# Kernel tuning notes

Measured on AMD Instinct MI355X. Metric: run time of the kernel, lower is better.

The kernel has to match this reference:

```python
import jax, jax.numpy as jnp
import numpy as np
import math

H = 14
W = 14
MU_MAX = math.sqrt((H / 2) ** 2 + (W / 2) ** 2)
EPS = 1e-6
LN_EPS = 1e-5


def _distance_sq():
    fy = np.fft.fftfreq(H) * H
    fx = np.fft.rfftfreq(W) * W
    d = fy[:, None] ** 2 + fx[None, :] ** 2  # (H, W//2+1)
    return jnp.asarray(d[None, None], dtype=jnp.float32)  # (1,1,H,W//2+1)


def setup_inputs() -> dict:
    key = jax.random.key(0)
    k0, k1, k2 = jax.random.split(key, 3)
    B, C, HID = 256, 768, 192  # hidden = max(768//4, 8)
    return {
        "x": jax.random.normal(k0, (B, 197, C), jnp.float32),
        "ln_gamma": jnp.ones((C,), jnp.float32),
        "ln_beta": jnp.zeros((C,), jnp.float32),
        "w1": jax.random.normal(k1, (C, HID), jnp.float32) * 0.02,
        "b1": jnp.zeros((HID,), jnp.float32),
        "w2": jax.random.normal(k2, (HID, 2), jnp.float32) * 0.02,
        "b2": jnp.zeros((2,), jnp.float32),
        "residual_scale": jnp.asarray(1e-4, jnp.float32),
    }


def reference(x, ln_gamma, ln_beta, w1, b1, w2, b2, residual_scale):
    b, _, c = x.shape
    cls_tok = x[:, :1]          # (B,1,C)
    xs = x[:, 1:]               # (B,196,C) raw spatial tokens
    # LayerNorm (biased variance, eps=1e-5 like torch default)
    mu_ln = xs.mean(-1, keepdims=True)
    var_ln = xs.var(-1, keepdims=True)
    xn = (xs - mu_ln) / jnp.sqrt(var_ln + LN_EPS) * ln_gamma + ln_beta
    # to (B,C,H,W) grid
    xg = xn.transpose(0, 2, 1).reshape(b, c, H, W)
    xm = xg.mean((-2, -1), keepdims=True)
    spec = jnp.fft.rfft2(xg - xm, norm='ortho')  # (B,C,H,W//2+1) complex
    energy = jnp.log1p(jnp.abs(spec)).mean((-2, -1))  # (B,C)
    hdn = jax.nn.gelu(energy @ w1 + b1, approximate=False)
    out2 = hdn @ w2 + b2  # (B,2)
    mu = jnp.maximum(MU_MAX * jax.nn.sigmoid(out2[:, 0]), 1.0).reshape(b, 1, 1, 1)
    sigma = jnp.maximum(jax.nn.softplus(out2[:, 1]), 0.1).reshape(b, 1, 1, 1)
    mask = jnp.exp(-_distance_sq() / (2.0 * mu ** 2 * sigma + EPS))
    filtered = jnp.fft.irfft2(spec * mask, s=(H, W), norm='ortho') + xm
    toks = filtered.reshape(b, c, H * W).transpose(0, 2, 1)  # (B,196,C)
    delta = toks - xn
    return jnp.concatenate([cls_tok, xs + residual_scale * delta], axis=1)
```

## Files before the change

kernel.cpp:

```cpp
#include <hip/hip_runtime.h>
#include <hip/hip_fp16.h>
#include <math.h>

#define NB    256
#define NTOKP 197
#define NTOK  196
#define NC    768
#define NHID  192
#define NH    14
#define NVF   8
#define CHT   64
#define NTILE 12
#define NCH   8
#define CCH   (NC / NCH)

constexpr float CT14[14] = {
    1.0f, 0.9009688679024191f, 0.6234898018587336f, 0.22252093395631445f,
    -0.22252093395631434f, -0.6234898018587335f, -0.9009688679024191f, -1.0f,
    -0.9009688679024191f, -0.6234898018587335f, -0.22252093395631434f,
    0.22252093395631445f, 0.6234898018587336f, 0.9009688679024191f};
constexpr float ST14[14] = {
    0.0f, 0.4338837391175581f, 0.7818314824680298f, 0.9749279121818236f,
    0.9749279121818236f, 0.7818314824680299f, 0.43388373911755823f, 0.0f,
    -0.43388373911755823f, -0.7818314824680299f, -0.9749279121818236f,
    -0.9749279121818236f, -0.7818314824680298f, -0.4338837391175581f};

__device__ __forceinline__ unsigned int h2bits(__half2 h) {
  return *(unsigned int*)&h;
}

template <bool WH>
__global__ __launch_bounds__(256) void k_stats(const float* __restrict__ x,
                                               const float* __restrict__ gamma,
                                               const float* __restrict__ beta,
                                               float2* __restrict__ msv,
                                               __half* __restrict__ xnh) {
  int row = blockIdx.x * 4 + (threadIdx.x >> 6);
  int lane = threadIdx.x & 63;
  if (row >= NB * NTOK) return;
  int b = row / NTOK, t = row - b * NTOK;
  const float4* p = (const float4*)(x + ((size_t)b * NTOKP + 1 + t) * NC);
  float4 v[3];
  float s = 0.f, ss = 0.f;
#pragma unroll
  for (int k = 0; k < 3; ++k) {
    v[k] = p[lane + k * 64];
    s += v[k].x + v[k].y + v[k].z + v[k].w;
    ss += v[k].x * v[k].x + v[k].y * v[k].y + v[k].z * v[k].z + v[k].w * v[k].w;
  }
#pragma unroll
  for (int m = 32; m; m >>= 1) {
    s += __shfl_xor(s, m);
    ss += __shfl_xor(ss, m);
  }
  float mean = s * (1.f / NC);
  float var = ss * (1.f / NC) - mean * mean;
  float rstd = rsqrtf(var + 1e-5f);
  if (lane == 0) msv[row] = make_float2(mean, rstd);
  if (WH) {
#pragma unroll
    for (int k = 0; k < 3; ++k) {
      float4 g = ((const float4*)gamma)[lane + k * 64];
      float4 be = ((const float4*)beta)[lane + k * 64];
      float4 xn;
      xn.x = (v[k].x - mean) * rstd * g.x + be.x;
      xn.y = (v[k].y - mean) * rstd * g.y + be.y;
      xn.z = (v[k].z - mean) * rstd * g.z + be.z;
      xn.w = (v[k].w - mean) * rstd * g.w + be.w;
      uint2 u = make_uint2(h2bits(__floats2half2_rn(xn.x, xn.y)),
                           h2bits(__floats2half2_rn(xn.z, xn.w)));
      *(uint2*)(xnh + (size_t)row * NC + lane * 4 + k * 256) = u;
    }
  }
}

template <bool UH>
__global__ __launch_bounds__(256) void k_fwd(const float* __restrict__ x,
                                             const __half* __restrict__ xnh,
                                             const float* __restrict__ gamma,
                                             const float* __restrict__ beta,
                                             const float2* __restrict__ msv,
                                             float* __restrict__ energy) {
  __shared__ __half2 A[NH * NVF * CHT];
  __shared__ float2 ms[UH ? 1 : NTOK];
  __shared__ float esum[256];
  int b = blockIdx.y, c0 = blockIdx.x * CHT, tid = threadIdx.x;
  int c = tid & 63, w = tid >> 6;

  float g = 0.f, be = 0.f;
  if (!UH) {
    for (int k = tid; k < NTOK; k += 256) ms[k] = msv[b * NTOK + k];
    g = gamma[c0 + c];
    be = beta[c0 + c];
  }

  __half2 TW1[14], TW2[14];
#pragma unroll
  for (int k = 0; k < 14; ++k) {
    TW1[k] = __floats2half2_rn(CT14[k], -ST14[k]);
    TW2[k] = __floats2half2_rn(ST14[k], CT14[k]);
  }
  __syncthreads();

#pragma unroll 1
  for (int i = w; i < NH; i += 4) {
    __half2 xh[NH];
    if (UH) {
      const __half* xr = xnh + ((size_t)b * NTOK + i * NH) * NC + c0 + c;
#pragma unroll
      for (int j = 0; j < NH; ++j) xh[j] = __half2half2(xr[(size_t)j * NC]);
    } else {
      const float* xr = x + ((size_t)b * NTOKP + 1 + i * NH) * NC + c0 + c;
#pragma unroll
      for (int j = 0; j < NH; ++j) {
        float2 m = ms[i * NH + j];
        xh[j] = __float2half2_rn((xr[(size_t)j * NC] - m.x) * m.y * g + be);
      }
    }
    __half2 acc[NVF];
#pragma unroll
    for (int v = 0; v < NVF; ++v) acc[v] = __floats2half2_rn(0.f, 0.f);
#pragma unroll
    for (int j = 0; j < NH; ++j) {
#pragma unroll
      for (int v = 0; v < NVF; ++v)
        acc[v] = __hfma2(xh[j], TW1[(v * j) % 14], acc[v]);
    }
#pragma unroll
    for (int v = 0; v < NVF; ++v) A[(i * NVF + v) * CHT + c] = acc[v];
  }
  __syncthreads();

  float part = 0.f;
#pragma unroll 1
  for (int vv = 0; vv < 2; ++vv) {
    int v = w * 2 + vv;
    bool herm = (v == 0) || (v == 7);
    const __half2* Ac = A + v * CHT + c;
    __half2 E[7], O[7];
#pragma unroll
    for (int k = 0; k < 7; ++k) {
      E[k] = __floats2half2_rn(0.f, 0.f);
      O[k] = __floats2half2_rn(0.f, 0.f);
    }
#pragma unroll
    for (int m = 0; m < 7; ++m) {
      __half2 ae = Ac[(2 * m) * NVF * CHT];
      __half2 ao = Ac[(2 * m + 1) * NVF * CHT];
      __half2 aer = __low2half2(ae), aei = __high2half2(ae);
      __half2 aor = __low2half2(ao), aoi = __high2half2(ao);
#pragma unroll
      for (int k = 0; k < 7; ++k) {
        int t = (2 * k * m) % 14;
        E[k] = __hfma2(aer, TW1[t], __hfma2(aei, TW2[t], E[k]));
        O[k] = __hfma2(aor, TW1[t], __hfma2(aoi, TW2[t], O[k]));
      }
    }
    float pa = 1.f, pb = 1.f;
#pragma unroll
    for (int u = 0; u < 14; ++u) {
      if (!herm || u < 8) {
        int k = u % 7;
        __half2 Ov = O[k];
        __half2 S = __hfma2(__low2half2(Ov), TW1[u],
                            __hfma2(__high2half2(Ov), TW2[u], E[k]));
        float2 s2 = __half22float2(S);
        float mag = 14.f + __builtin_amdgcn_sqrtf(fmaf(s2.x, s2.x, s2.y * s2.y));
        if (herm) {
          float msq = mag * mag;
          if (u == 0) {
            if (v == 7) pb *= mag;
          } else if (u <= 3) {
            pa *= msq;
          } else if (u <= 6) {
            pb *= msq;
          } else {
            pb *= mag;
          }
        } else {
          if (u < 7) pa *= mag; else pb *= mag;
        }
      }
    }
    part += __logf(pa) + __logf(pb);
  }
  esum[tid] = part;
  __syncthreads();
  if (w == 0) {
    float e = esum[c] + esum[c + 64] + esum[c + 128] + esum[c + 192];
    energy[(size_t)b * NC + c0 + c] =
        (e - 111.f * 2.6390573296152584f) * (1.f / 112.f);
  }
}

__global__ __launch_bounds__(192) void k_mlp1(const float* __restrict__ energy,
                                              const float* __restrict__ w1,
                                              float* __restrict__ partial) {
  int s = blockIdx.x, b = blockIdx.y;
  int h = threadIdx.x;
  const float* ep = energy + (size_t)b * NC + s * CCH;
  const float* wp = w1 + (size_t)s * CCH * NHID + h;
  float acc = 0.f;
#pragma unroll 8
  for (int cc = 0; cc < CCH; ++cc)
    acc = fmaf(ep[cc], wp[(size_t)cc * NHID], acc);
  partial[((size_t)b * NCH + s) * NHID + h] = acc;
}

__global__ __launch_bounds__(192) void k_final(const float* __restrict__ partial,
                                               const float* __restrict__ b1,
                                               const float* __restrict__ w2,
                                               const float* __restrict__ b2,
                                               float* __restrict__ m2s) {
  __shared__ float2 sh[NHID];
  int b = blockIdx.x, h = threadIdx.x;
  float a = b1[h];
#pragma unroll
  for (int s = 0; s < NCH; ++s) a += partial[((size_t)b * NCH + s) * NHID + h];
  float ge = 0.5f * a * (1.f + erff(a * 0.70710678118654752f));
  sh[h] = make_float2(ge * w2[2 * h], ge * w2[2 * h + 1]);
  __syncthreads();
  if (h < 64) {
    float p0 = sh[h].x + sh[h + 64].x + sh[h + 128].x;
    float p1 = sh[h].y + sh[h + 64].y + sh[h + 128].y;
#pragma unroll
    for (int off = 32; off; off >>= 1) {
      p0 += __shfl_down(p0, off);
      p1 += __shfl_down(p1, off);
    }
    if (h == 0) {
      float o0 = p0 + b2[0], o1 = p1 + b2[1];
      float muv = 9.899494936611665f / (1.f + expf(-o0));
      muv = fmaxf(muv, 1.f);
      float sp = (o1 > 20.f) ? o1 : log1pf(expf(o1));
      float sg = fmaxf(sp, 0.1f);
      m2s[b] = 2.f * muv * muv * sg + 1e-6f;
    }
  }
}

template <bool UH>
__global__ __launch_bounds__(256) void k_inv(const float* __restrict__ x,
                                             const __half* __restrict__ xnh,
                                             const float* __restrict__ gamma,
                                             const float* __restrict__ beta,
                                             const float2* __restrict__ msv,
                                             const float* __restrict__ m2s,
                                             const float* __restrict__ rscale,
                                             float* __restrict__ out) {
  __shared__ __half2 T[NH * 7 * CHT];
  __shared__ float2 ms[NTOK];
  __shared__ float rr[UH ? NTOK : 1];
  __shared__ float wexp[NH];
  __shared__ float kc[NH];
  int b = blockIdx.y, c0 = blockIdx.x * CHT, tid = threadIdx.x;
  int c = tid & 63, w = tid >> 6;
  float rs = rscale[0];

  for (int k = tid; k < NTOK; k += 256) {
    float2 m = msv[b * NTOK + k];
    ms[k] = m;
    if (UH) rr[k] = 1.f / m.y;
  }
  if (tid < CHT) {
    size_t idx = (size_t)b * NTOKP * NC + c0 + tid;
    out[idx] = x[idx];
  }
  float msb = m2s[b];
  if (tid < NH) {
    int f = (tid <= 7) ? tid : 14 - tid;
    wexp[tid] = __expf(-(float)(f * f) / msb);
  }
  __syncthreads();
  if (tid < NH) {
    float s = 0.f;
#pragma unroll
    for (int k = 0; k < NH; ++k) s = fmaf(wexp[k], CT14[(k * tid) % 14], s);
    kc[tid] = s * (1.f / 14.f);
  }
  float g = gamma[c0 + c], be = beta[c0 + c];
  float rg = 1.f / g;
  __syncthreads();

  float kr[NH];
#pragma unroll
  for (int d = 0; d < NH; ++d) kr[d] = kc[d];
  __half2 khp[NH];
#pragma unroll
  for (int d = 0; d < NH; ++d) khp[d] = __floats2half2_rn(kr[d], kr[(d + 1) % 14]);

#pragma unroll 1
  for (int i = w; i < NH; i += 4) {
    __half2 xh[NH];
    if (UH) {
      const __half* xr = xnh + ((size_t)b * NTOK + i * NH) * NC + c0 + c;
#pragma unroll
      for (int j = 0; j < NH; ++j) xh[j] = __half2half2(xr[(size_t)j * NC]);
    } else {
      const float* xr = x + ((size_t)b * NTOKP + 1 + i * NH) * NC + c0 + c;
#pragma unroll
      for (int j = 0; j < NH; ++j) {
        float2 m = ms[i * NH + j];
        xh[j] = __float2half2_rn((xr[(size_t)j * NC] - m.x) * m.y * g + be);
      }
    }
#pragma unroll
    for (int jp = 0; jp < 7; ++jp) {
      __half2 acc = __floats2half2_rn(0.f, 0.f);
#pragma unroll
      for (int j = 0; j < NH; ++j)
        acc = __hfma2(xh[j], khp[(2 * jp - j + 28) % 14], acc);
      T[(i * 7 + jp) * CHT + c] = acc;
    }
  }
  __syncthreads();

#pragma unroll 1
  for (int jq = w; jq < NH; jq += 4) {
    int jp = jq >> 1, hi = jq & 1;
    __half2 acc2[7];
#pragma unroll
    for (int d = 0; d < 7; ++d) acc2[d] = __floats2half2_rn(0.f, 0.f);
#pragma unroll
    for (int i = 0; i < NH; ++i) {
      __half2 t = T[(i * 7 + jp) * CHT + c];
      __half2 yi = hi ? __high2half2(t) : __low2half2(t);
#pragma unroll
      for (int d = 0; d < 7; ++d)
        acc2[d] = __hfma2(yi, khp[(2 * d - i + 28) % 14], acc2[d]);
    }
    float* outr = out + ((size_t)b * NTOKP + 1 + jq) * NC + c0 + c;
    const __half* xq = xnh + ((size_t)b * NTOK + jq) * NC + c0 + c;
    const float* xr = x + ((size_t)b * NTOKP + 1 + jq) * NC + c0 + c;
#pragma unroll
    for (int ii = 0; ii < NH; ++ii) {
      float z = (ii & 1) ? __high2float(acc2[ii >> 1]) : __low2float(acc2[ii >> 1]);
      if (UH) {
        float xnv = __half2float(xq[(size_t)ii * NH * NC]);
        int t = ii * NH + jq;
        float xv = fmaf((xnv - be) * rg, rr[t], ms[t].x);
        outr[(size_t)ii * NH * NC] = xv + rs * (z - xnv);
      } else {
        float xv = xr[(size_t)ii * NH * NC];
        float2 m = ms[ii * NH + jq];
        float xn = (xv - m.x) * m.y * g + be;
        outr[(size_t)ii * NH * NC] = xv + rs * (z - xn);
      }
    }
  }
}

extern "C" void kernel_launch(void* const* d_in, const int* in_sizes, int n_in,
                              void* d_out, int out_size, void* d_ws, size_t ws_size,
                              hipStream_t stream) {
  (void)in_sizes; (void)n_in; (void)out_size;
  const float* x      = (const float*)d_in[0];
  const float* gamma  = (const float*)d_in[1];
  const float* beta   = (const float*)d_in[2];
  const float* w1     = (const float*)d_in[3];
  const float* b1     = (const float*)d_in[4];
  const float* w2     = (const float*)d_in[5];
  const float* b2     = (const float*)d_in[6];
  const float* rscale = (const float*)d_in[7];
  float* out = (float*)d_out;

  char* wsb = (char*)d_ws;
  float2* msv = (float2*)(wsb + 0);
  float* m2s  = (float*)(wsb + 401408);
  __half* xnh = (__half*)(wsb + 402432);
  size_t need = 402432 + (size_t)NB * NTOK * NC * 2;
  bool useH = ws_size >= need;

  float* energy  = (float*)((char*)d_out + 150994944);
  float* partial = (float*)((char*)d_out + 152043520);

  if (useH) {
    k_stats<true><<<NB * NTOK / 4, 256, 0, stream>>>(x, gamma, beta, msv, xnh);
    k_fwd<true><<<dim3(NTILE, NB), 256, 0, stream>>>(x, xnh, gamma, beta, msv,
                                                     energy);
  } else {
    k_stats<false><<<NB * NTOK / 4, 256, 0, stream>>>(x, gamma, beta, msv, xnh);
    k_fwd<false><<<dim3(NTILE, NB), 256, 0, stream>>>(x, xnh, gamma, beta, msv,
                                                      energy);
  }
  k_mlp1<<<dim3(NCH, NB), 192, 0, stream>>>(energy, w1, partial);
  k_final<<<NB, 192, 0, stream>>>(partial, b1, w2, b2, m2s);
  if (useH) {
    k_inv<true><<<dim3(NTILE, NB), 256, 0, stream>>>(x, xnh, gamma, beta, msv,
                                                     m2s, rscale, out);
  } else {
    k_inv<false><<<dim3(NTILE, NB), 256, 0, stream>>>(x, xnh, gamma, beta, msv,
                                                      m2s, rscale, out);
  }
}
```

Before: 140.6 us.

## Fuse MLP first layer into forward kernel and MLP tail into inverse kernel

```diff
diff --git a/kernel.cpp b/kernel.cpp
--- a/kernel.cpp
+++ b/kernel.cpp
@@ -11,8 +11,6 @@
 #define NVF   8
 #define CHT   64
 #define NTILE 12
-#define NCH   8
-#define CCH   (NC / NCH)
 
 constexpr float CT14[14] = {
     1.0f, 0.9009688679024191f, 0.6234898018587336f, 0.22252093395631445f,
@@ -80,10 +78,12 @@
                                              const float* __restrict__ gamma,
                                              const float* __restrict__ beta,
                                              const float2* __restrict__ msv,
-                                             float* __restrict__ energy) {
+                                             const float* __restrict__ w1,
+                                             __half* __restrict__ partial) {
   __shared__ __half2 A[NH * NVF * CHT];
   __shared__ float2 ms[UH ? 1 : NTOK];
   __shared__ float esum[256];
+  __shared__ float el[CHT];
   int b = blockIdx.y, c0 = blockIdx.x * CHT, tid = threadIdx.x;
   int c = tid & 63, w = tid >> 6;
 
@@ -188,54 +188,15 @@
   __syncthreads();
   if (w == 0) {
     float e = esum[c] + esum[c + 64] + esum[c + 128] + esum[c + 192];
-    energy[(size_t)b * NC + c0 + c] =
-        (e - 111.f * 2.6390573296152584f) * (1.f / 112.f);
-  }
-}
-
-__global__ __launch_bounds__(192) void k_mlp1(const float* __restrict__ energy,
-                                              const float* __restrict__ w1,
-                                              float* __restrict__ partial) {
-  int s = blockIdx.x, b = blockIdx.y;
-  int h = threadIdx.x;
-  const float* ep = energy + (size_t)b * NC + s * CCH;
-  const float* wp = w1 + (size_t)s * CCH * NHID + h;
-  float acc = 0.f;
+    el[c] = (e - 111.f * 2.6390573296152584f) * (1.f / 112.f);
+  }
+  __syncthreads();
+  if (tid < NHID) {
+    float acc = 0.f;
 #pragma unroll 8
-  for (int cc = 0; cc < CCH; ++cc)
-    acc = fmaf(ep[cc], wp[(size_t)cc * NHID], acc);
-  partial[((size_t)b * NCH + s) * NHID + h] = acc;
-}
-
-__global__ __launch_bounds__(192) void k_final(const float* __restrict__ partial,
-                                               const float* __restrict__ b1,
-                                               const float* __restrict__ w2,
-                                               const float* __restrict__ b2,
-                                               float* __restrict__ m2s) {
-  __shared__ float2 sh[NHID];
-  int b = blockIdx.x, h = threadIdx.x;
-  float a = b1[h];
-#pragma unroll
-  for (int s = 0; s < NCH; ++s) a += partial[((size_t)b * NCH + s) * NHID + h];
-  float ge = 0.5f * a * (1.f + erff(a * 0.70710678118654752f));
-  sh[h] = make_float2(ge * w2[2 * h], ge * w2[2 * h + 1]);
-  __syncthreads();
-  if (h < 64) {
-    float p0 = sh[h].x + sh[h + 64].x + sh[h + 128].x;
-    float p1 = sh[h].y + sh[h + 64].y + sh[h + 128].y;
-#pragma unroll
-    for (int off = 32; off; off >>= 1) {
-      p0 += __shfl_down(p0, off);
-      p1 += __shfl_down(p1, off);
-    }
-    if (h == 0) {
-      float o0 = p0 + b2[0], o1 = p1 + b2[1];
-      float muv = 9.899494936611665f / (1.f + expf(-o0));
-      muv = fmaxf(muv, 1.f);
-      float sp = (o1 > 20.f) ? o1 : log1pf(expf(o1));
-      float sg = fmaxf(sp, 0.1f);
-      m2s[b] = 2.f * muv * muv * sg + 1e-6f;
-    }
+    for (int cc = 0; cc < CHT; ++cc)
+      acc = fmaf(el[cc], w1[(size_t)(c0 + cc) * NHID + tid], acc);
+    partial[((size_t)b * NTILE + blockIdx.x) * NHID + tid] = __float2half(acc);
   }
 }
 
@@ -245,7 +206,10 @@
                                              const float* __restrict__ gamma,
                                              const float* __restrict__ beta,
                                              const float2* __restrict__ msv,
-                                             const float* __restrict__ m2s,
+                                             const __half* __restrict__ partial,
+                                             const float* __restrict__ b1,
+                                             const float* __restrict__ w2,
+                                             const float* __restrict__ b2,
                                              const float* __restrict__ rscale,
                                              float* __restrict__ out) {
   __shared__ __half2 T[NH * 7 * CHT];
@@ -253,6 +217,8 @@
   __shared__ float rr[UH ? NTOK : 1];
   __shared__ float wexp[NH];
   __shared__ float kc[NH];
+  __shared__ float2 sh2[NHID];
+  __shared__ float msb_sh;
   int b = blockIdx.y, c0 = blockIdx.x * CHT, tid = threadIdx.x;
   int c = tid & 63, w = tid >> 6;
   float rs = rscale[0];
@@ -266,7 +232,33 @@
     size_t idx = (size_t)b * NTOKP * NC + c0 + tid;
     out[idx] = x[idx];
   }
-  float msb = m2s[b];
+  if (tid < NHID) {
+    float a = b1[tid];
+#pragma unroll
+    for (int s = 0; s < NTILE; ++s)
+      a += __half2float(partial[((size_t)b * NTILE + s) * NHID + tid]);
+    float ge = 0.5f * a * (1.f + erff(a * 0.70710678118654752f));
+    sh2[tid] = make_float2(ge * w2[2 * tid], ge * w2[2 * tid + 1]);
+  }
+  __syncthreads();
+  if (tid < 64) {
+    float p0 = sh2[tid].x + sh2[tid + 64].x + sh2[tid + 128].x;
+    float p1 = sh2[tid].y + sh2[tid + 64].y + sh2[tid + 128].y;
+#pragma unroll
+    for (int off = 32; off; off >>= 1) {
+      p0 += __shfl_down(p0, off);
+      p1 += __shfl_down(p1, off);
+    }
+    if (tid == 0) {
+      float o0 = p0 + b2[0], o1 = p1 + b2[1];
+      float muv = fmaxf(9.899494936611665f / (1.f + expf(-o0)), 1.f);
+      float sp = (o1 > 20.f) ? o1 : log1pf(expf(o1));
+      float sg = fmaxf(sp, 0.1f);
+      msb_sh = 2.f * muv * muv * sg + 1e-6f;
+    }
+  }
+  __syncthreads();
+  float msb = msb_sh;
   if (tid < NH) {
     int f = (tid <= 7) ? tid : 14 - tid;
     wexp[tid] = __expf(-(float)(f * f) / msb);
@@ -365,31 +357,25 @@
   float* out = (float*)d_out;
 
   char* wsb = (char*)d_ws;
-  float2* msv = (float2*)(wsb + 0);
-  float* m2s  = (float*)(wsb + 401408);
-  __half* xnh = (__half*)(wsb + 402432);
-  size_t need = 402432 + (size_t)NB * NTOK * NC * 2;
+  float2* msv     = (float2*)(wsb + 0);
+  __half* partial = (__half*)(wsb + 401408);
+  __half* xnh     = (__half*)(wsb + 1581056);
+  size_t need = 1581056 + (size_t)NB * NTOK * NC * 2;
   bool useH = ws_size >= need;
-
-  float* energy  = (float*)((char*)d_out + 150994944);
-  float* partial = (float*)((char*)d_out + 152043520);
 
   if (useH) {
     k_stats<true><<<NB * NTOK / 4, 256, 0, stream>>>(x, gamma, beta, msv, xnh);
     k_fwd<true><<<dim3(NTILE, NB), 256, 0, stream>>>(x, xnh, gamma, beta, msv,
-                                                     energy);
+                                                     w1, partial);
+    k_inv<true><<<dim3(NTILE, NB), 256, 0, stream>>>(x, xnh, gamma, beta, msv,
+                                                     partial, b1, w2, b2,
+                                                     rscale, out);
   } else {
     k_stats<false><<<NB * NTOK / 4, 256, 0, stream>>>(x, gamma, beta, msv, xnh);
     k_fwd<false><<<dim3(NTILE, NB), 256, 0, stream>>>(x, xnh, gamma, beta, msv,
-                                                      energy);
-  }
-  k_mlp1<<<dim3(NCH, NB), 192, 0, stream>>>(energy, w1, partial);
-  k_final<<<NB, 192, 0, stream>>>(partial, b1, w2, b2, m2s);
-  if (useH) {
-    k_inv<true><<<dim3(NTILE, NB), 256, 0, stream>>>(x, xnh, gamma, beta, msv,
-                                                     m2s, rscale, out);
-  } else {
+                                                      w1, partial);
     k_inv<false><<<dim3(NTILE, NB), 256, 0, stream>>>(x, xnh, gamma, beta, msv,
-                                                      m2s, rscale, out);
-  }
-}
+                                                      partial, b1, w2, b2,
+                                                      rscale, out);
+  }
+}
```

Result: faster. 137.1 us, median of 2 (-2.5%).
